# Kernel tuning notes

Measured on AMD Instinct MI355X. Metric: run time of the kernel, lower is better.

Reference implementation:

```python
import jax, jax.numpy as jnp
import numpy as np

SEQ_LEN, BATCH, INPUT, HIDDEN, OUTPUT = 2048, 64, 256, 256, 256


def setup_inputs() -> dict:
    key = jax.random.key(0)
    ks = jax.random.split(key, 6)
    return {
        "inputs": jax.random.normal(ks[0], (SEQ_LEN, BATCH, INPUT), dtype=jnp.float32),
        "h0": jnp.zeros((BATCH, HIDDEN), dtype=jnp.float32),
        "Wh": jax.random.normal(ks[1], (HIDDEN, HIDDEN), dtype=jnp.float32),
        "Ux": jax.random.normal(ks[2], (INPUT, HIDDEN), dtype=jnp.float32),
        "bh": jax.random.normal(ks[3], (HIDDEN,), dtype=jnp.float32),
        "Vo": jax.random.normal(ks[4], (HIDDEN, OUTPUT), dtype=jnp.float32),
        "co": jax.random.normal(ks[5], (OUTPUT,), dtype=jnp.float32),
    }


def reference(inputs, h0, Wh, Ux, bh, Vo, co):
    # Precompute the input projection for all timesteps in one big GEMM:
    # (S, B, I) @ (I, H) -> (S, B, H). The recurrence itself is a scan.
    x_proj = jnp.einsum("sbi,ih->sbh", inputs, Ux) + bh

    def step(ht, xp_t):
        ht_new = jnp.tanh(xp_t + ht @ Wh)   # (B, H)
        ot = ht_new @ Vo + co               # (B, O)
        return ht_new, ot

    ht_final, outputs = jax.lax.scan(step, h0, x_proj)
    return outputs, ht_final
```

## Files before the change

### kernel.cpp

```cpp
#include <hip/hip_runtime.h>
#include <math.h>


#define SEQ 2048
#define BATCH 64
#define HID 256
#define BH 16384

__device__ __forceinline__ float tanh_xla(float x) {
  const float kClamp = 7.99881172180175781f;
  float xc = fminf(fmaxf(x, -kClamp), kClamp);
  float x2 = __fmul_rn(xc, xc);
  float p = __fmaf_rn(x2, -2.76076847742355e-16f, 2.00018790482477e-13f);
  p = __fmaf_rn(x2, p, -8.60467152213735e-11f);
  p = __fmaf_rn(x2, p, 5.12229709037114e-08f);
  p = __fmaf_rn(x2, p, 1.48572235717979e-05f);
  p = __fmaf_rn(x2, p, 6.37261928875436e-04f);
  p = __fmaf_rn(x2, p, 4.89352455891786e-03f);
  p = __fmul_rn(xc, p);
  float q = __fmaf_rn(x2, 1.19825839466702e-06f, 1.18534705686654e-04f);
  q = __fmaf_rn(x2, q, 2.26843463243900e-03f);
  q = __fmaf_rn(x2, q, 4.89352518554385e-03f);
  float r = __fdiv_rn(p, q);
  return (fabsf(x) < 0.0004f) ? x : r;
}

__global__ __launch_bounds__(256) void xp_dot_kernel(
    const float* __restrict__ X, const float* __restrict__ Ux,
    const float* __restrict__ bh, float* __restrict__ XP) {
  __shared__ float xs[8][256];

  const int tid = threadIdx.x;
  const size_t row0 = (size_t)blockIdx.x * 8;

  const float4* src = (const float4*)(X + row0 * 256);
  float4* dst = (float4*)&xs[0][0];
  dst[tid] = src[tid];
  dst[256 + tid] = src[256 + tid];
  __syncthreads();

  const int h = tid;
  float acc[8] = {0.f, 0.f, 0.f, 0.f, 0.f, 0.f, 0.f, 0.f};

#pragma unroll 4
  for (int i = 0; i < 256; ++i) {
    float u = Ux[i * 256 + h];
#pragma unroll
    for (int r = 0; r < 8; ++r)
      acc[r] = __fmaf_rn(xs[r][i], u, acc[r]);
  }

  const float b = bh[h];
#pragma unroll
  for (int r = 0; r < 8; ++r)
    XP[(row0 + r) * 256 + h] = __fadd_rn(acc[r], b);
}

#define WLD(K) { float wt = Wh[(K) * 256 + j]; \
  asm volatile("v_accvgpr_write_b32 a" #K ", %0" :: "v"(wt) : "a" #K); }
#define WLD4(K0,K1,K2,K3) WLD(K0) WLD(K1) WLD(K2) WLD(K3)

#define WR1(K, D) asm volatile("v_accvgpr_read_b32 %0, a" #K : "=v"(D));

#define GRPF(HB, CW0,CW1,CW2,CW3, NK0,NK1,NK2,NK3, NW0,NW1,NW2,NW3, NQ) { \
  acc = __fmaf_rn(HB.x, CW0, acc); WR1(NK0, NW0) \
  acc = __fmaf_rn(HB.y, CW1, acc); WR1(NK1, NW1) \
  acc = __fmaf_rn(HB.z, CW2, acc); WR1(NK2, NW2) \
  acc = __fmaf_rn(HB.w, CW3, acc); WR1(NK3, NW3) \
  HB = h4[NQ]; }

#define GRPN(HB, CW0,CW1,CW2,CW3, NK0,NK1,NK2,NK3, NW0,NW1,NW2,NW3) { \
  acc = __fmaf_rn(HB.x, CW0, acc); WR1(NK0, NW0) \
  acc = __fmaf_rn(HB.y, CW1, acc); WR1(NK1, NW1) \
  acc = __fmaf_rn(HB.z, CW2, acc); WR1(NK2, NW2) \
  acc = __fmaf_rn(HB.w, CW3, acc); WR1(NK3, NW3) }

#define GRPE(HB, CW0,CW1,CW2,CW3) { \
  acc = __fmaf_rn(HB.x, CW0, acc); \
  acc = __fmaf_rn(HB.y, CW1, acc); \
  acc = __fmaf_rn(HB.z, CW2, acc); \
  acc = __fmaf_rn(HB.w, CW3, acc); }

__global__ __launch_bounds__(256)
__attribute__((amdgpu_waves_per_eu(1, 1)))
void scan_xla_kernel(
    const float* __restrict__ Wh, const float* __restrict__ h0,
    float* __restrict__ xpH, float* __restrict__ hfinal) {
  __shared__ float hbuf0[256];
  __shared__ float hbuf1[256];

  const int b = blockIdx.x;
  const int j = threadIdx.x;

  WLD4(0,1,2,3)       WLD4(4,5,6,7)       WLD4(8,9,10,11)     WLD4(12,13,14,15)
  WLD4(16,17,18,19)   WLD4(20,21,22,23)   WLD4(24,25,26,27)   WLD4(28,29,30,31)
  WLD4(32,33,34,35)   WLD4(36,37,38,39)   WLD4(40,41,42,43)   WLD4(44,45,46,47)
  WLD4(48,49,50,51)   WLD4(52,53,54,55)   WLD4(56,57,58,59)   WLD4(60,61,62,63)
  WLD4(64,65,66,67)   WLD4(68,69,70,71)   WLD4(72,73,74,75)   WLD4(76,77,78,79)
  WLD4(80,81,82,83)   WLD4(84,85,86,87)   WLD4(88,89,90,91)   WLD4(92,93,94,95)
  WLD4(96,97,98,99)   WLD4(100,101,102,103) WLD4(104,105,106,107) WLD4(108,109,110,111)
  WLD4(112,113,114,115) WLD4(116,117,118,119) WLD4(120,121,122,123) WLD4(124,125,126,127)
  WLD4(128,129,130,131) WLD4(132,133,134,135) WLD4(136,137,138,139) WLD4(140,141,142,143)
  WLD4(144,145,146,147) WLD4(148,149,150,151) WLD4(152,153,154,155) WLD4(156,157,158,159)
  WLD4(160,161,162,163) WLD4(164,165,166,167) WLD4(168,169,170,171) WLD4(172,173,174,175)
  WLD4(176,177,178,179) WLD4(180,181,182,183) WLD4(184,185,186,187) WLD4(188,189,190,191)
  WLD4(192,193,194,195) WLD4(196,197,198,199) WLD4(200,201,202,203) WLD4(204,205,206,207)
  WLD4(208,209,210,211) WLD4(212,213,214,215) WLD4(216,217,218,219) WLD4(220,221,222,223)
  WLD4(224,225,226,227) WLD4(228,229,230,231) WLD4(232,233,234,235) WLD4(236,237,238,239)
  WLD4(240,241,242,243) WLD4(244,245,246,247) WLD4(248,249,250,251) WLD4(252,253,254,255)

  hbuf0[j] = h0[b * 256 + j];
  __syncthreads();

  float xp_cur = xpH[(size_t)b * 256 + j];
  float hn_prev = 0.f;
  const float* cur = hbuf0;
  float* nxt = hbuf1;

  for (int t = 0; t < SEQ; ++t) {
    if (t > 0)
      xpH[(size_t)(t - 1) * BH + b * 256 + j] = hn_prev;
    float xp_next = (t + 1 < SEQ) ? xpH[(size_t)(t + 1) * BH + b * 256 + j] : 0.f;

    const float4* h4 = (const float4*)cur;
    float4 hb0 = h4[0], hb1 = h4[1], hb2 = h4[2], hb3 = h4[3];
    float4 hb4 = h4[4], hb5 = h4[5], hb6 = h4[6], hb7 = h4[7];

    float wa0, wa1, wa2, wa3, wb0, wb1, wb2, wb3;
    WR1(0, wa0) WR1(1, wa1) WR1(2, wa2) WR1(3, wa3)

    float acc = 0.f;
    GRPF(hb0, wa0,wa1,wa2,wa3,   4,5,6,7,     wb0,wb1,wb2,wb3,  8)
    GRPF(hb1, wb0,wb1,wb2,wb3,   8,9,10,11,   wa0,wa1,wa2,wa3,  9)
    GRPF(hb2, wa0,wa1,wa2,wa3,   12,13,14,15, wb0,wb1,wb2,wb3, 10)
    GRPF(hb3, wb0,wb1,wb2,wb3,   16,17,18,19, wa0,wa1,wa2,wa3, 11)
    GRPF(hb4, wa0,wa1,wa2,wa3,   20,21,22,23, wb0,wb1,wb2,wb3, 12)
    GRPF(hb5, wb0,wb1,wb2,wb3,   24,25,26,27, wa0,wa1,wa2,wa3, 13)
    GRPF(hb6, wa0,wa1,wa2,wa3,   28,29,30,31, wb0,wb1,wb2,wb3, 14)
    GRPF(hb7, wb0,wb1,wb2,wb3,   32,33,34,35, wa0,wa1,wa2,wa3, 15)
    GRPF(hb0, wa0,wa1,wa2,wa3,   36,37,38,39, wb0,wb1,wb2,wb3, 16)
    GRPF(hb1, wb0,wb1,wb2,wb3,   40,41,42,43, wa0,wa1,wa2,wa3, 17)
    GRPF(hb2, wa0,wa1,wa2,wa3,   44,45,46,47, wb0,wb1,wb2,wb3, 18)
    GRPF(hb3, wb0,wb1,wb2,wb3,   48,49,50,51, wa0,wa1,wa2,wa3, 19)
    GRPF(hb4, wa0,wa1,wa2,wa3,   52,53,54,55, wb0,wb1,wb2,wb3, 20)
    GRPF(hb5, wb0,wb1,wb2,wb3,   56,57,58,59, wa0,wa1,wa2,wa3, 21)
    GRPF(hb6, wa0,wa1,wa2,wa3,   60,61,62,63, wb0,wb1,wb2,wb3, 22)
    GRPF(hb7, wb0,wb1,wb2,wb3,   64,65,66,67, wa0,wa1,wa2,wa3, 23)
    GRPF(hb0, wa0,wa1,wa2,wa3,   68,69,70,71, wb0,wb1,wb2,wb3, 24)
    GRPF(hb1, wb0,wb1,wb2,wb3,   72,73,74,75, wa0,wa1,wa2,wa3, 25)
    GRPF(hb2, wa0,wa1,wa2,wa3,   76,77,78,79, wb0,wb1,wb2,wb3, 26)
    GRPF(hb3, wb0,wb1,wb2,wb3,   80,81,82,83, wa0,wa1,wa2,wa3, 27)
    GRPF(hb4, wa0,wa1,wa2,wa3,   84,85,86,87, wb0,wb1,wb2,wb3, 28)
    GRPF(hb5, wb0,wb1,wb2,wb3,   88,89,90,91, wa0,wa1,wa2,wa3, 29)
    GRPF(hb6, wa0,wa1,wa2,wa3,   92,93,94,95, wb0,wb1,wb2,wb3, 30)
    GRPF(hb7, wb0,wb1,wb2,wb3,   96,97,98,99, wa0,wa1,wa2,wa3, 31)
    GRPF(hb0, wa0,wa1,wa2,wa3,   100,101,102,103, wb0,wb1,wb2,wb3, 32)
    GRPF(hb1, wb0,wb1,wb2,wb3,   104,105,106,107, wa0,wa1,wa2,wa3, 33)
    GRPF(hb2, wa0,wa1,wa2,wa3,   108,109,110,111, wb0,wb1,wb2,wb3, 34)
    GRPF(hb3, wb0,wb1,wb2,wb3,   112,113,114,115, wa0,wa1,wa2,wa3, 35)
    GRPF(hb4, wa0,wa1,wa2,wa3,   116,117,118,119, wb0,wb1,wb2,wb3, 36)
    GRPF(hb5, wb0,wb1,wb2,wb3,   120,121,122,123, wa0,wa1,wa2,wa3, 37)
    GRPF(hb6, wa0,wa1,wa2,wa3,   124,125,126,127, wb0,wb1,wb2,wb3, 38)
    GRPF(hb7, wb0,wb1,wb2,wb3,   128,129,130,131, wa0,wa1,wa2,wa3, 39)
    GRPF(hb0, wa0,wa1,wa2,wa3,   132,133,134,135, wb0,wb1,wb2,wb3, 40)
    GRPF(hb1, wb0,wb1,wb2,wb3,   136,137,138,139, wa0,wa1,wa2,wa3, 41)
    GRPF(hb2, wa0,wa1,wa2,wa3,   140,141,142,143, wb0,wb1,wb2,wb3, 42)
    GRPF(hb3, wb0,wb1,wb2,wb3,   144,145,146,147, wa0,wa1,wa2,wa3, 43)
    GRPF(hb4, wa0,wa1,wa2,wa3,   148,149,150,151, wb0,wb1,wb2,wb3, 44)
    GRPF(hb5, wb0,wb1,wb2,wb3,   152,153,154,155, wa0,wa1,wa2,wa3, 45)
    GRPF(hb6, wa0,wa1,wa2,wa3,   156,157,158,159, wb0,wb1,wb2,wb3, 46)
    GRPF(hb7, wb0,wb1,wb2,wb3,   160,161,162,163, wa0,wa1,wa2,wa3, 47)
    GRPF(hb0, wa0,wa1,wa2,wa3,   164,165,166,167, wb0,wb1,wb2,wb3, 48)
    GRPF(hb1, wb0,wb1,wb2,wb3,   168,169,170,171, wa0,wa1,wa2,wa3, 49)
    GRPF(hb2, wa0,wa1,wa2,wa3,   172,173,174,175, wb0,wb1,wb2,wb3, 50)
    GRPF(hb3, wb0,wb1,wb2,wb3,   176,177,178,179, wa0,wa1,wa2,wa3, 51)
    GRPF(hb4, wa0,wa1,wa2,wa3,   180,181,182,183, wb0,wb1,wb2,wb3, 52)
    GRPF(hb5, wb0,wb1,wb2,wb3,   184,185,186,187, wa0,wa1,wa2,wa3, 53)
    GRPF(hb6, wa0,wa1,wa2,wa3,   188,189,190,191, wb0,wb1,wb2,wb3, 54)
    GRPF(hb7, wb0,wb1,wb2,wb3,   192,193,194,195, wa0,wa1,wa2,wa3, 55)
    GRPF(hb0, wa0,wa1,wa2,wa3,   196,197,198,199, wb0,wb1,wb2,wb3, 56)
    GRPF(hb1, wb0,wb1,wb2,wb3,   200,201,202,203, wa0,wa1,wa2,wa3, 57)
    GRPF(hb2, wa0,wa1,wa2,wa3,   204,205,206,207, wb0,wb1,wb2,wb3, 58)
    GRPF(hb3, wb0,wb1,wb2,wb3,   208,209,210,211, wa0,wa1,wa2,wa3, 59)
    GRPF(hb4, wa0,wa1,wa2,wa3,   212,213,214,215, wb0,wb1,wb2,wb3, 60)
    GRPF(hb5, wb0,wb1,wb2,wb3,   216,217,218,219, wa0,wa1,wa2,wa3, 61)
    GRPF(hb6, wa0,wa1,wa2,wa3,   220,221,222,223, wb0,wb1,wb2,wb3, 62)
    GRPF(hb7, wb0,wb1,wb2,wb3,   224,225,226,227, wa0,wa1,wa2,wa3, 63)
    GRPN(hb0, wa0,wa1,wa2,wa3,   228,229,230,231, wb0,wb1,wb2,wb3)
    GRPN(hb1, wb0,wb1,wb2,wb3,   232,233,234,235, wa0,wa1,wa2,wa3)
    GRPN(hb2, wa0,wa1,wa2,wa3,   236,237,238,239, wb0,wb1,wb2,wb3)
    GRPN(hb3, wb0,wb1,wb2,wb3,   240,241,242,243, wa0,wa1,wa2,wa3)
    GRPN(hb4, wa0,wa1,wa2,wa3,   244,245,246,247, wb0,wb1,wb2,wb3)
    GRPN(hb5, wb0,wb1,wb2,wb3,   248,249,250,251, wa0,wa1,wa2,wa3)
    GRPN(hb6, wa0,wa1,wa2,wa3,   252,253,254,255, wb0,wb1,wb2,wb3)
    GRPE(hb7, wb0,wb1,wb2,wb3)

    float z = __fadd_rn(xp_cur, acc);
    float hn = tanh_xla(z);

    nxt[j] = hn;
    __syncthreads();

    const float* tmp = cur; cur = nxt; nxt = (float*)tmp;
    xp_cur = xp_next;
    hn_prev = hn;
  }

  xpH[(size_t)(SEQ - 1) * BH + b * 256 + j] = hn_prev;
  hfinal[b * 256 + j] = hn_prev;
}

__global__ __launch_bounds__(256) void gemm_inplace_kernel(
    float* __restrict__ HO, const float* __restrict__ Vo,
    const float* __restrict__ co) {
  __shared__ float Hs[64][260];
  __shared__ float Bs[32][64];

  const int tid = threadIdx.x;
  const int bm = blockIdx.x;
  float* base = HO + (size_t)bm * 64 * 256;

#pragma unroll
  for (int l = 0; l < 16; ++l) {
    int idx = l * 256 + tid;
    int r = idx >> 6;
    int c4 = idx & 63;
    float4 v = *(const float4*)&base[r * 256 + c4 * 4];
    *(float4*)&Hs[r][c4 * 4] = v;
  }

  const int tr = tid >> 4;
  const int tc = tid & 15;

  for (int bn = 0; bn < 4; ++bn) {
    float acc[4][4];
#pragma unroll
    for (int i = 0; i < 4; ++i)
#pragma unroll
      for (int jj = 0; jj < 4; ++jj) acc[i][jj] = 0.f;

    for (int kt = 0; kt < 256; kt += 32) {
      __syncthreads();
#pragma unroll
      for (int l = 0; l < 2; ++l) {
        int idx = tid * 2 + l;
        int k2 = idx >> 4;
        int nn = (idx & 15) << 2;
        float4 bv = *(const float4*)&Vo[(size_t)(kt + k2) * 256 + bn * 64 + nn];
        *(float4*)&Bs[k2][nn] = bv;
      }
      __syncthreads();
#pragma unroll
      for (int k = 0; k < 32; ++k) {
        float4 bq = *(const float4*)&Bs[k][tc * 4];
        float bv[4] = {bq.x, bq.y, bq.z, bq.w};
#pragma unroll
        for (int i = 0; i < 4; ++i) {
          float a = Hs[tr * 4 + i][kt + k];
#pragma unroll
          for (int jj = 0; jj < 4; ++jj) acc[i][jj] += a * bv[jj];
        }
      }
    }

    const float4 cb = *(const float4*)&co[bn * 64 + tc * 4];
    const float cv[4] = {cb.x, cb.y, cb.z, cb.w};
#pragma unroll
    for (int i = 0; i < 4; ++i) {
      float4 o;
      o.x = acc[i][0] + cv[0];
      o.y = acc[i][1] + cv[1];
      o.z = acc[i][2] + cv[2];
      o.w = acc[i][3] + cv[3];
      *(float4*)&base[(tr * 4 + i) * 256 + bn * 64 + tc * 4] = o;
    }
  }
}

extern "C" void kernel_launch(void* const* d_in, const int* in_sizes, int n_in,
                              void* d_out, int out_size, void* d_ws, size_t ws_size,
                              hipStream_t stream) {
  const float* inputs = (const float*)d_in[0];
  const float* h0     = (const float*)d_in[1];
  const float* Wh     = (const float*)d_in[2];
  const float* Ux     = (const float*)d_in[3];
  const float* bh     = (const float*)d_in[4];
  const float* Vo     = (const float*)d_in[5];
  const float* co     = (const float*)d_in[6];

  float* out = (float*)d_out;
  float* hfinal = out + (size_t)SEQ * BATCH * 256;
  (void)d_ws; (void)ws_size;

  const int M = SEQ * BATCH;

  xp_dot_kernel<<<M / 8, 256, 0, stream>>>(inputs, Ux, bh, out);

  scan_xla_kernel<<<BATCH, 256, 0, stream>>>(Wh, h0, out, hfinal);

  gemm_inplace_kernel<<<M / 64, 256, 0, stream>>>(out, Vo, co);
}
```

Baseline: 3.807 ms.

## Add streaming scan kernel that re-reads Wh from cache each step, two batches per block

```diff
diff --git a/kernel.cpp b/kernel.cpp
--- a/kernel.cpp
+++ b/kernel.cpp
@@ -54,6 +54,93 @@
 #pragma unroll
   for (int r = 0; r < 8; ++r)
     XP[(row0 + r) * 256 + h] = __fadd_rn(acc[r], b);
+}
+
+__global__ __launch_bounds__(512, 2)
+void scan_stream_kernel(
+    const float* __restrict__ Wh, const float* __restrict__ h0,
+    float* __restrict__ xpH, float* __restrict__ hfinal) {
+  __shared__ float hbuf0[2][256];
+  __shared__ float hbuf1[2][256];
+
+  const int tid = threadIdx.x;
+  const int rr = tid >> 8;
+  const int j = tid & 255;
+  const int b = blockIdx.x * 2 + rr;
+
+  float wq0[8], wq1[8], wq2[8], wq3[8];
+
+  hbuf0[rr][j] = h0[b * 256 + j];
+  __syncthreads();
+
+  float xp_cur = xpH[(size_t)b * 256 + j];
+  float hn_prev = 0.f;
+  const float* cur = hbuf0[rr];
+  float* nxt = hbuf1[rr];
+
+  uintptr_t wpb = (uintptr_t)Wh;
+
+  {
+    const float* whp = (const float*)wpb;
+#pragma unroll
+    for (int q = 0; q < 8; ++q) wq0[q] = whp[(0 * 8 + q) * 256 + j];
+#pragma unroll
+    for (int q = 0; q < 8; ++q) wq1[q] = whp[(1 * 8 + q) * 256 + j];
+#pragma unroll
+    for (int q = 0; q < 8; ++q) wq2[q] = whp[(2 * 8 + q) * 256 + j];
+  }
+
+  for (int t = 0; t < SEQ; ++t) {
+    asm volatile("" : "+s"(wpb));
+    const float* whp = (const float*)wpb;
+
+    if (t > 0)
+      xpH[(size_t)(t - 1) * BH + b * 256 + j] = hn_prev;
+    float xp_next = (t + 1 < SEQ) ? xpH[(size_t)(t + 1) * BH + b * 256 + j] : 0.f;
+
+    float acc = 0.f;
+    const float4* h4 = (const float4*)cur;
+
+#define PHASE(C, LB, UB)                                                      \
+    {                                                                         \
+      _Pragma("unroll")                                                       \
+      for (int q = 0; q < 8; ++q)                                             \
+        LB[q] = whp[((((C) + 3) & 31) * 8 + q) * 256 + j];                    \
+      float4 hv = h4[(C) * 2];                                                \
+      acc = __fmaf_rn(hv.x, UB[0], acc);                                      \
+      acc = __fmaf_rn(hv.y, UB[1], acc);                                      \
+      acc = __fmaf_rn(hv.z, UB[2], acc);                                      \
+      acc = __fmaf_rn(hv.w, UB[3], acc);                                      \
+      hv = h4[(C) * 2 + 1];                                                   \
+      acc = __fmaf_rn(hv.x, UB[4], acc);                                      \
+      acc = __fmaf_rn(hv.y, UB[5], acc);                                      \
+      acc = __fmaf_rn(hv.z, UB[6], acc);                                      \
+      acc = __fmaf_rn(hv.w, UB[7], acc);                                      \
+    }
+
+    PHASE(0,  wq3, wq0) PHASE(1,  wq0, wq1) PHASE(2,  wq1, wq2) PHASE(3,  wq2, wq3)
+    PHASE(4,  wq3, wq0) PHASE(5,  wq0, wq1) PHASE(6,  wq1, wq2) PHASE(7,  wq2, wq3)
+    PHASE(8,  wq3, wq0) PHASE(9,  wq0, wq1) PHASE(10, wq1, wq2) PHASE(11, wq2, wq3)
+    PHASE(12, wq3, wq0) PHASE(13, wq0, wq1) PHASE(14, wq1, wq2) PHASE(15, wq2, wq3)
+    PHASE(16, wq3, wq0) PHASE(17, wq0, wq1) PHASE(18, wq1, wq2) PHASE(19, wq2, wq3)
+    PHASE(20, wq3, wq0) PHASE(21, wq0, wq1) PHASE(22, wq1, wq2) PHASE(23, wq2, wq3)
+    PHASE(24, wq3, wq0) PHASE(25, wq0, wq1) PHASE(26, wq1, wq2) PHASE(27, wq2, wq3)
+    PHASE(28, wq3, wq0) PHASE(29, wq0, wq1) PHASE(30, wq1, wq2) PHASE(31, wq2, wq3)
+#undef PHASE
+
+    float z = __fadd_rn(xp_cur, acc);
+    float hn = tanh_xla(z);
+
+    nxt[j] = hn;
+    __syncthreads();
+
+    const float* tmp = cur; cur = nxt; nxt = (float*)tmp;
+    xp_cur = xp_next;
+    hn_prev = hn;
+  }
+
+  xpH[(size_t)(SEQ - 1) * BH + b * 256 + j] = hn_prev;
+  hfinal[b * 256 + j] = hn_prev;
 }
 
 #define WLD(K) { float wt = Wh[(K) * 256 + j]; \
@@ -296,7 +383,15 @@
 
   xp_dot_kernel<<<M / 8, 256, 0, stream>>>(inputs, Ux, bh, out);
 
-  scan_xla_kernel<<<BATCH, 256, 0, stream>>>(Wh, h0, out, hfinal);
+  hipFuncAttributes attr{};
+  bool use_stream = false;
+  if (hipFuncGetAttributes(&attr, (const void*)scan_stream_kernel) == hipSuccess)
+    use_stream = (attr.localSizeBytes == 0);
+
+  if (use_stream)
+    scan_stream_kernel<<<BATCH / 2, 512, 0, stream>>>(Wh, h0, out, hfinal);
+  else
+    scan_xla_kernel<<<BATCH, 256, 0, stream>>>(Wh, h0, out, hfinal);
 
   gemm_inplace_kernel<<<M / 64, 256, 0, stream>>>(out, Vo, co);
 }
```

Measured after the change: 11.74 ms. 3.08x slower.
